# Kernel optimization log

Hardware: AMD Instinct MI355X
Metric: run time of the kernel (lower is better)

The kernel has to match this reference:

```python
import jax, jax.numpy as jnp
import numpy as np

N = 50000
E = 400000
DIM_IN = 512
DIM_H = 64
HEADS = 8
DIM_OUT = 40
SLOPE = 0.2  # PyG GATv2Conv default negative_slope


def setup_inputs() -> dict:
    key = jax.random.key(0)
    ks = jax.random.split(key, 16)
    s = 0.05
    return {
        "x": jax.random.normal(ks[0], (N, DIM_IN), dtype=jnp.float32),
        "edge_index": jax.random.randint(ks[1], (2, E), 0, N, dtype=jnp.int64),
        "Wl1": jax.random.normal(ks[2], (DIM_IN, HEADS * DIM_H), dtype=jnp.float32) * s,
        "Wr1": jax.random.normal(ks[3], (DIM_IN, HEADS * DIM_H), dtype=jnp.float32) * s,
        "att1": jax.random.normal(ks[4], (HEADS, DIM_H), dtype=jnp.float32) * s,
        "b1": jax.random.normal(ks[5], (HEADS * DIM_H,), dtype=jnp.float32) * s,
        "Wl2": jax.random.normal(ks[6], (HEADS * DIM_H, DIM_OUT), dtype=jnp.float32) * s,
        "Wr2": jax.random.normal(ks[7], (HEADS * DIM_H, DIM_OUT), dtype=jnp.float32) * s,
        "att2": jax.random.normal(ks[8], (1, DIM_OUT), dtype=jnp.float32) * s,
        "b2": jax.random.normal(ks[9], (DIM_OUT,), dtype=jnp.float32) * s,
        "Wl3": jax.random.normal(ks[10], (HEADS * DIM_H, 2), dtype=jnp.float32) * s,
        "Wr3": jax.random.normal(ks[11], (HEADS * DIM_H, 2), dtype=jnp.float32) * s,
        "att3": jax.random.normal(ks[12], (1, 2), dtype=jnp.float32) * s,
        "b3": jax.random.normal(ks[13], (2,), dtype=jnp.float32) * s,
    }


def gatv2(x, src, dst, Wl, Wr, att, b):
    # PyG GATv2Conv: e_ij = att . LeakyReLU(W_l x_j + W_r x_i); softmax over j (by dst i);
    # out_i = sum_j alpha_ij * (W_l x_j); heads concatenated; bias added after.
    n = x.shape[0]
    H, F = att.shape
    xl = (x @ Wl).reshape(n, H, F)  # source transform
    xr = (x @ Wr).reshape(n, H, F)  # target transform
    e = jax.nn.leaky_relu(xl[src] + xr[dst], negative_slope=SLOPE)  # [E, H, F]
    logits = jnp.einsum("ehf,hf->eh", e, att)  # [E, H]
    m = jax.ops.segment_max(logits, dst, num_segments=n)  # self-loops => every segment nonempty
    ex = jnp.exp(logits - m[dst])
    denom = jax.ops.segment_sum(ex, dst, num_segments=n)
    alpha = ex / denom[dst]  # [E, H]
    out = jax.ops.segment_sum(xl[src] * alpha[:, :, None], dst, num_segments=n)  # [N, H, F]
    return out.reshape(n, H * F) + b


def reference(x, edge_index, Wl1, Wr1, att1, b1, Wl2, Wr2, att2, b2, Wl3, Wr3, att3, b3):
    # add self loops (PyG default add_self_loops=True)
    loops = jnp.arange(N, dtype=edge_index.dtype)
    ei = jnp.concatenate([edge_index, jnp.stack([loops, loops])], axis=1)
    src, dst = ei[0], ei[1]
    # eval mode: dropout is identity; ReverseLayerF is identity in forward
    h = jax.nn.relu(gatv2(x, src, dst, Wl1, Wr1, att1, b1))
    y_class = gatv2(h, src, dst, Wl2, Wr2, att2, b2)
    y_domain = gatv2(h, src, dst, Wl3, Wr3, att3, b3)
    return (y_class, y_domain)
```

## Files before the change

### kernel.cpp

```cpp
#include <hip/hip_runtime.h>
#include <math.h>

typedef unsigned short u16;
typedef unsigned int   u32;
typedef __attribute__((ext_vector_type(8))) short bf16x8;
typedef __attribute__((ext_vector_type(4))) float f32x4;
typedef __attribute__((ext_vector_type(4))) u32   u32x4;

__device__ __forceinline__ float b2f(u16 u) {
  union { u32 i; float f; } v; v.i = ((u32)u) << 16; return v.f;
}
__device__ __forceinline__ u16 f2b(float f) {
  union { u32 i; float f; } v; v.f = f;
  u32 r = v.i + 0x7FFFu + ((v.i >> 16) & 1u);
  return (u16)(r >> 16);
}
__device__ __forceinline__ float blo(u32 w) {
  union { u32 i; float f; } v; v.i = w << 16; return v.f;
}
__device__ __forceinline__ float bhi(u32 w) {
  union { u32 i; float f; } v; v.i = w & 0xFFFF0000u; return v.f;
}
__device__ __forceinline__ void ld_lds16(const u16* g, u16* l) {
  __builtin_amdgcn_global_load_lds((const __attribute__((address_space(1))) void*)g,
                                   (__attribute__((address_space(3))) void*)l, 16, 0, 0);
}

#define NN 50000
#define NE 400000
#define NT 450000
#define NBLK_SCAN 196

__global__ void k_detect(const void* x, const void* ei, int* flags) {
  __shared__ int cnt[2];
  int t = threadIdx.x;
  if (t < 2) cnt[t] = 0;
  __syncthreads();
  u16 u = ((const u16*)x)[t];
  int e = (u >> 7) & 0xFF;
  if (u == 0 || (e >= 90 && e <= 134)) atomicAdd(&cnt[0], 1);
  if (t < 16) {
    if (((const int*)ei)[2 * t + 1] == 0) atomicAdd(&cnt[1], 1);
  }
  __syncthreads();
  if (t == 0) {
    flags[0] = (cnt[0] >= 110) ? 1 : 0;
    flags[1] = (cnt[1] >= 15) ? 1 : 0;
  }
}

__device__ __forceinline__ int eidx(const int* ei, int pos, int i64) {
  return i64 ? ei[2 * pos] : ei[pos];
}

__global__ void k_convert_x(const void* x, const int* flags, u16* xb) {
  if (flags[0]) return;
  int c = blockIdx.x * 256 + threadIdx.x;
  const float* xf = (const float*)x + (size_t)c * 8;
  u32x4 o;
  #pragma unroll
  for (int i = 0; i < 4; ++i) {
    u32 lo = f2b(xf[2 * i]);
    u32 hi = f2b(xf[2 * i + 1]);
    o[i] = lo | (hi << 16);
  }
  *(u32x4*)(xb + (size_t)c * 8) = o;
}

__global__ void k_pack_w1t(const void* Wl1, const void* Wr1, const int* flags, u16* w1t) {
  int t = blockIdx.x * 256 + threadIdx.x;
  int k = t >> 10;
  int c = t & 1023;
  const void* W = (c < 512) ? Wl1 : Wr1;
  int cc = c & 511;
  u16 v;
  if (flags[0]) v = ((const u16*)W)[k * 512 + cc];
  else          v = f2b(((const float*)W)[k * 512 + cc]);
  w1t[c * 512 + k] = v;
}

__global__ void k_pack_w23t(const void* Wl2, const void* Wr2, const void* Wl3, const void* Wr3,
                            const int* flags, u16* w23t) {
  int t = blockIdx.x * 256 + threadIdx.x;
  int k = t / 96;
  int c = t % 96;
  const void* W = nullptr; int idx = 0;
  if (c < 40)      { W = Wl2; idx = k * 40 + c; }
  else if (c < 42) { W = Wl3; idx = k * 2 + (c - 40); }
  else if (c < 82) { W = Wr2; idx = k * 40 + (c - 42); }
  else if (c < 84) { W = Wr3; idx = k * 2 + (c - 82); }
  u16 v = 0;
  if (W) {
    if (flags[0]) v = ((const u16*)W)[idx];
    else          v = f2b(((const float*)W)[idx]);
  }
  w23t[c * 512 + k] = v;
}

__global__ void k_pack_params(const void* att1, const void* b1, const void* att2, const void* b2,
                              const void* att3, const void* b3, const int* flags, float* params) {
  int t = blockIdx.x * 256 + threadIdx.x;
  if (t >= 1108) return;
  const void* src; int idx;
  if (t < 512)       { src = att1; idx = t; }
  else if (t < 1024) { src = b1;   idx = t - 512; }
  else if (t < 1064) { src = att2; idx = t - 1024; }
  else if (t < 1104) { src = b2;   idx = t - 1064; }
  else if (t < 1106) { src = att3; idx = t - 1104; }
  else               { src = b3;   idx = t - 1106; }
  params[t] = flags[0] ? b2f(((const u16*)src)[idx]) : ((const float*)src)[idx];
}

__global__ void k_hist(const int* ei, const int* flags, int* deg) {
  int e = blockIdx.x * 256 + threadIdx.x;
  if (e >= NE) return;
  int d = eidx(ei, NE + e, flags[1]);
  atomicAdd(&deg[d], 1);
}

__global__ void k_scanA(const int* deg, int* row_ptr, int* bsum) {
  __shared__ int sh[256];
  int b = blockIdx.x, t = threadIdx.x;
  int i = b * 256 + t;
  int val = (i < NN) ? deg[i] + 1 : 0;
  sh[t] = val;
  __syncthreads();
  #pragma unroll
  for (int off = 1; off < 256; off <<= 1) {
    int v = (t >= off) ? sh[t - off] : 0;
    __syncthreads();
    sh[t] += v;
    __syncthreads();
  }
  if (i < NN) row_ptr[i] = sh[t] - val;
  if (t == 255) bsum[b] = sh[255];
}

__global__ void k_scanB(int* bsum, int* row_ptr) {
  __shared__ int sh[256];
  int t = threadIdx.x;
  int val = (t < NBLK_SCAN) ? bsum[t] : 0;
  sh[t] = val;
  __syncthreads();
  #pragma unroll
  for (int off = 1; off < 256; off <<= 1) {
    int v = (t >= off) ? sh[t - off] : 0;
    __syncthreads();
    sh[t] += v;
    __syncthreads();
  }
  if (t < NBLK_SCAN) bsum[t] = sh[t] - val;
  if (t == 255) row_ptr[NN] = sh[255];
}

__global__ void k_scanC(const int* bsum, int* row_ptr, int* cursor) {
  int i = blockIdx.x * 256 + threadIdx.x;
  if (i < NN) {
    int v = row_ptr[i] + bsum[blockIdx.x];
    row_ptr[i] = v;
    cursor[i] = v;
  }
}

__global__ void k_scatter(const int* ei, const int* flags, int* cursor, int* csr_src) {
  int t = blockIdx.x * 256 + threadIdx.x;
  if (t >= NT) return;
  int i64 = flags[1];
  int s, d;
  if (t < NE) { s = eidx(ei, t, i64); d = eidx(ei, NE + t, i64); }
  else        { s = d = t - NE; }
  int pos = atomicAdd(&cursor[d], 1);
  csr_src[pos] = s;
}

__global__ __launch_bounds__(256) void k_gemm1(const void* __restrict__ xraw, const u16* __restrict__ xb,
                                               const u16* __restrict__ Bt, const int* __restrict__ flags,
                                               u16* __restrict__ XL, u16* __restrict__ XR) {
  __shared__ __align__(16) u16 As[128 * 64];
  __shared__ __align__(16) u16 Bs[128 * 64];
  const int id  = blockIdx.x;
  const int xcd = id & 7;
  const int lb  = id >> 3;
  const int mt  = xcd * 49 + (lb >> 3);
  const int nt  = lb & 7;
  if (mt >= 391) return;
  const int m0 = mt * 128;
  const int n0 = nt * 128;
  const u16* __restrict__ A = flags[0] ? (const u16*)xraw : xb;
  const int t = threadIdx.x;
  const int wave = t >> 6;
  const int lane = t & 63;
  const int wm = (wave >> 1) * 64;
  const int wn = (wave & 1) * 64;
  const int fr = lane & 15;
  const int fk = lane >> 4;
  const int srow = lane >> 3;
  const int schk = (lane & 7) ^ srow;
  f32x4 acc[4][4] = {};
  for (int k0 = 0; k0 < 512; k0 += 64) {
    #pragma unroll
    for (int q = 0; q < 4; ++q) {
      int rbase = wave * 32 + q * 8;
      int gm = m0 + rbase + srow;
      if (gm > NN - 1) gm = NN - 1;
      ld_lds16(&A[(size_t)gm * 512 + k0 + schk * 8], &As[rbase * 64]);
      ld_lds16(&Bt[(size_t)(n0 + rbase + srow) * 512 + k0 + schk * 8], &Bs[rbase * 64]);
    }
    __syncthreads();
    #pragma unroll
    for (int h = 0; h < 2; ++h) {
      int s = h * 4 + fk;
      bf16x8 af[4], bb[4];
      #pragma unroll
      for (int i = 0; i < 4; ++i) {
        int row = wm + i * 16 + fr;
        af[i] = *(const bf16x8*)&As[row * 64 + ((s ^ (row & 7)) * 8)];
      }
      #pragma unroll
      for (int j = 0; j < 4; ++j) {
        int row = wn + j * 16 + fr;
        bb[j] = *(const bf16x8*)&Bs[row * 64 + ((s ^ (row & 7)) * 8)];
      }
      #pragma unroll
      for (int i = 0; i < 4; ++i)
        #pragma unroll
        for (int j = 0; j < 4; ++j)
          acc[i][j] = __builtin_amdgcn_mfma_f32_16x16x32_bf16(af[i], bb[j], acc[i][j], 0, 0, 0);
    }
    __syncthreads();
  }
  #pragma unroll
  for (int i = 0; i < 4; ++i) {
    #pragma unroll
    for (int r = 0; r < 4; ++r) {
      int gm = m0 + wm + i * 16 + fk * 4 + r;
      if (gm < NN) {
        #pragma unroll
        for (int j = 0; j < 4; ++j) {
          int gn = n0 + wn + j * 16 + fr;
          u16 v = f2b(acc[i][j][r]);
          if (gn < 512) XL[(size_t)gm * 512 + gn] = v;
          else          XR[(size_t)gm * 512 + gn - 512] = v;
        }
      }
    }
  }
}

__global__ __launch_bounds__(256) void k_gemm2(const u16* __restrict__ A, const u16* __restrict__ Bt,
                                               float* __restrict__ C) {
  __shared__ __align__(16) short As[128][40];
  __shared__ __align__(16) short Bs[96][40];
  const int m0 = blockIdx.x * 128;
  const int t = threadIdx.x;
  const int wave = t >> 6;
  const int lane = t & 63;
  const int fr = lane & 15;
  const int fk = lane >> 4;
  const int wm = wave * 32;
  f32x4 acc[2][6] = {};
  for (int k0 = 0; k0 < 512; k0 += 32) {
    #pragma unroll
    for (int h = 0; h < 2; ++h) {
      int c = t + h * 256;
      int row = c >> 2, kc = (c & 3) * 8;
      int gm = m0 + row;
      u32x4 va = {0, 0, 0, 0};
      if (gm < NN) va = *(const u32x4*)&A[(size_t)gm * 512 + k0 + kc];
      *(u32x4*)&As[row][kc] = va;
    }
    for (int c = t; c < 384; c += 256) {
      int row = c >> 2, kc = (c & 3) * 8;
      *(u32x4*)&Bs[row][kc] = *(const u32x4*)&Bt[row * 512 + k0 + kc];
    }
    __syncthreads();
    bf16x8 af[2], bb[6];
    #pragma unroll
    for (int i = 0; i < 2; ++i) af[i] = *(const bf16x8*)&As[wm + i * 16 + fr][fk * 8];
    #pragma unroll
    for (int j = 0; j < 6; ++j) bb[j] = *(const bf16x8*)&Bs[j * 16 + fr][fk * 8];
    #pragma unroll
    for (int i = 0; i < 2; ++i)
      #pragma unroll
      for (int j = 0; j < 6; ++j)
        acc[i][j] = __builtin_amdgcn_mfma_f32_16x16x32_bf16(af[i], bb[j], acc[i][j], 0, 0, 0);
    __syncthreads();
  }
  #pragma unroll
  for (int i = 0; i < 2; ++i) {
    #pragma unroll
    for (int j = 0; j < 6; ++j) {
      int gn = j * 16 + fr;
      if (gn < 84) {
        #pragma unroll
        for (int r = 0; r < 4; ++r) {
          int gm = m0 + wm + i * 16 + fk * 4 + r;
          if (gm < NN) C[(size_t)gm * 84 + gn] = acc[i][j][r];
        }
      }
    }
  }
}

__global__ __launch_bounds__(256) void k_layer1f(const u16* __restrict__ xl1, const u16* __restrict__ xr1,
                                                 const int* __restrict__ row_ptr, const int* __restrict__ csr_src,
                                                 const float* __restrict__ params, u16* __restrict__ hb) {
  int wid = blockIdx.x * 4 + (threadIdx.x >> 6);
  int lane = threadIdx.x & 63;
  int nw = gridDim.x * 4;
  float att[8];
  #pragma unroll
  for (int k = 0; k < 8; ++k) att[k] = params[lane * 8 + k];
  for (int i = wid; i < NN; i += nw) {
    int e0 = row_ptr[i], e1 = row_ptr[i + 1];
    u32x4 xrv = *(const u32x4*)&xr1[(size_t)i * 512 + lane * 8];
    float xr[8];
    #pragma unroll
    for (int q = 0; q < 4; ++q) { xr[2 * q] = blo(xrv[q]); xr[2 * q + 1] = bhi(xrv[q]); }
    float s = 0.f;
    float acc[8] = {0.f, 0.f, 0.f, 0.f, 0.f, 0.f, 0.f, 0.f};
    int q0 = csr_src[e0];
    int q1 = csr_src[e0 + 1 < e1 ? e0 + 1 : e1 - 1];
    int q2 = csr_src[e0 + 2 < e1 ? e0 + 2 : e1 - 1];
    int q3 = csr_src[e0 + 3 < e1 ? e0 + 3 : e1 - 1];
    for (int p = e0; p < e1; p += 4) {
      int j0 = q0, j1 = q1, j2 = q2, j3 = q3;
      u32x4 v0 = *(const u32x4*)&xl1[(size_t)j0 * 512 + lane * 8];
      u32x4 v1 = *(const u32x4*)&xl1[(size_t)j1 * 512 + lane * 8];
      u32x4 v2 = *(const u32x4*)&xl1[(size_t)j2 * 512 + lane * 8];
      u32x4 v3 = *(const u32x4*)&xl1[(size_t)j3 * 512 + lane * 8];
      int np = p + 4;
      if (np < e1) {
        q0 = csr_src[np];
        q1 = csr_src[np + 1 < e1 ? np + 1 : e1 - 1];
        q2 = csr_src[np + 2 < e1 ? np + 2 : e1 - 1];
        q3 = csr_src[np + 3 < e1 ? np + 3 : e1 - 1];
      }
      float m1 = (p + 1 < e1) ? 1.f : 0.f;
      float m2 = (p + 2 < e1) ? 1.f : 0.f;
      float m3 = (p + 3 < e1) ? 1.f : 0.f;
      float c0 = 0.f, c1 = 0.f, c2 = 0.f, c3 = 0.f;
      float xlv0[8], xlv1[8], xlv2[8], xlv3[8];
      #pragma unroll
      for (int q = 0; q < 4; ++q) {
        xlv0[2 * q] = blo(v0[q]); xlv0[2 * q + 1] = bhi(v0[q]);
        xlv1[2 * q] = blo(v1[q]); xlv1[2 * q + 1] = bhi(v1[q]);
        xlv2[2 * q] = blo(v2[q]); xlv2[2 * q + 1] = bhi(v2[q]);
        xlv3[2 * q] = blo(v3[q]); xlv3[2 * q + 1] = bhi(v3[q]);
      }
      #pragma unroll
      for (int k = 0; k < 8; ++k) {
        float t0 = xlv0[k] + xr[k];
        float t1 = xlv1[k] + xr[k];
        float t2 = xlv2[k] + xr[k];
        float t3 = xlv3[k] + xr[k];
        c0 = fmaf(att[k], fmaxf(t0, 0.2f * t0), c0);
        c1 = fmaf(att[k], fmaxf(t1, 0.2f * t1), c1);
        c2 = fmaf(att[k], fmaxf(t2, 0.2f * t2), c2);
        c3 = fmaf(att[k], fmaxf(t3, 0.2f * t3), c3);
      }
      c0 += __shfl_xor(c0, 1, 64); c1 += __shfl_xor(c1, 1, 64);
      c2 += __shfl_xor(c2, 1, 64); c3 += __shfl_xor(c3, 1, 64);
      c0 += __shfl_xor(c0, 2, 64); c1 += __shfl_xor(c1, 2, 64);
      c2 += __shfl_xor(c2, 2, 64); c3 += __shfl_xor(c3, 2, 64);
      c0 += __shfl_xor(c0, 4, 64); c1 += __shfl_xor(c1, 4, 64);
      c2 += __shfl_xor(c2, 4, 64); c3 += __shfl_xor(c3, 4, 64);
      float pv0 = __expf(fminf(fmaxf(c0, -30.f), 30.f));
      float pv1 = __expf(fminf(fmaxf(c1, -30.f), 30.f)) * m1;
      float pv2 = __expf(fminf(fmaxf(c2, -30.f), 30.f)) * m2;
      float pv3 = __expf(fminf(fmaxf(c3, -30.f), 30.f)) * m3;
      s += (pv0 + pv1) + (pv2 + pv3);
      #pragma unroll
      for (int k = 0; k < 8; ++k) {
        float a = fmaf(pv0, xlv0[k], pv1 * xlv1[k]);
        float b = fmaf(pv2, xlv2[k], pv3 * xlv3[k]);
        acc[k] += a + b;
      }
    }
    float r = 1.f / s;
    u32x4 o;
    #pragma unroll
    for (int q = 0; q < 4; ++q) {
      u32 lo = f2b(fmaxf(fmaf(acc[2 * q],     r, params[512 + lane * 8 + 2 * q]),     0.f));
      u32 hi = f2b(fmaxf(fmaf(acc[2 * q + 1], r, params[512 + lane * 8 + 2 * q + 1]), 0.f));
      o[q] = lo | (hi << 16);
    }
    *(u32x4*)&hb[(size_t)i * 512 + lane * 8] = o;
  }
}

__global__ __launch_bounds__(256) void k_layer23f(const float* __restrict__ xlr23, const int* __restrict__ row_ptr,
                                                  const int* __restrict__ csr_src, const float* __restrict__ params,
                                                  const int* __restrict__ flags, void* __restrict__ out) {
  int wid = blockIdx.x * 4 + (threadIdx.x >> 6);
  int lane = threadIdx.x & 63;
  int nw = gridDim.x * 4;
  int c = lane;
  bool act = c < 42;
  float att = 0.f;
  if (c < 40)      att = params[1024 + c];
  else if (c < 42) att = params[1104 + (c - 40)];
  int isbf = flags[0];
  for (int i = wid; i < NN; i += nw) {
    int e0 = row_ptr[i], e1 = row_ptr[i + 1];
    float xr = act ? xlr23[(size_t)i * 84 + 42 + c] : 0.f;
    float s2 = 0.f, s3 = 0.f, acc = 0.f;
    for (int p = e0; p < e1; p += 2) {
      int p1 = p + 1 < e1 ? p + 1 : e1 - 1;
      float m1 = (p + 1 < e1) ? 1.f : 0.f;
      int j0 = csr_src[p], j1 = csr_src[p1];
      float xl0 = act ? xlr23[(size_t)j0 * 84 + c] : 0.f;
      float xl1 = act ? xlr23[(size_t)j1 * 84 + c] : 0.f;
      float t0 = xl0 + xr, t1 = xl1 + xr;
      float v0 = att * fmaxf(t0, 0.2f * t0);
      float v1 = att * fmaxf(t1, 0.2f * t1);
      float w0 = (c < 40) ? v0 : 0.f;
      float w1 = (c < 40) ? v1 : 0.f;
      #pragma unroll
      for (int o = 32; o >= 1; o >>= 1) { w0 += __shfl_xor(w0, o, 64); w1 += __shfl_xor(w1, o, 64); }
      float u0 = v0 + __shfl_xor(v0, 1, 64);
      float u1 = v1 + __shfl_xor(v1, 1, 64);
      float l3_0 = __shfl(u0, 40, 64);
      float l3_1 = __shfl(u1, 40, 64);
      float p2_0 = __expf(fminf(fmaxf(w0, -30.f), 30.f));
      float p2_1 = __expf(fminf(fmaxf(w1, -30.f), 30.f)) * m1;
      float p3_0 = __expf(fminf(fmaxf(l3_0, -30.f), 30.f));
      float p3_1 = __expf(fminf(fmaxf(l3_1, -30.f), 30.f)) * m1;
      s2 += p2_0 + p2_1;
      s3 += p3_0 + p3_1;
      float a0 = (c < 40) ? p2_0 : p3_0;
      float a1 = (c < 40) ? p2_1 : p3_1;
      acc += fmaf(a0, xl0, a1 * xl1);
    }
    if (c < 40) {
      float v = acc / s2 + params[1064 + c];
      size_t o = (size_t)i * 40 + c;
      if (isbf) ((u16*)out)[o] = f2b(v); else ((float*)out)[o] = v;
    } else if (c < 42) {
      float v = acc / s3 + params[1106 + (c - 40)];
      size_t o = 2000000 + (size_t)i * 2 + (c - 40);
      if (isbf) ((u16*)out)[o] = f2b(v); else ((float*)out)[o] = v;
    }
  }
}

extern "C" void kernel_launch(void* const* d_in, const int* in_sizes, int n_in,
                              void* d_out, int out_size, void* d_ws, size_t ws_size,
                              hipStream_t stream) {
  const void* x    = d_in[0];
  const int*  ei   = (const int*)d_in[1];
  const void* Wl1  = d_in[2];
  const void* Wr1  = d_in[3];
  const void* att1 = d_in[4];
  const void* b1   = d_in[5];
  const void* Wl2  = d_in[6];
  const void* Wr2  = d_in[7];
  const void* att2 = d_in[8];
  const void* b2   = d_in[9];
  const void* Wl3  = d_in[10];
  const void* Wr3  = d_in[11];
  const void* att3 = d_in[12];
  const void* b3   = d_in[13];
  (void)in_sizes; (void)n_in; (void)out_size;

  char* ws = (char*)d_ws;
  size_t off = 0;
  auto alloc = [&](size_t bytes) -> void* {
    void* p = ws + off;
    off = (off + bytes + 255) & ~(size_t)255;
    return p;
  };
  int*   flags   = (int*)  alloc(64);
  u16*   xb      = (u16*)  alloc((size_t)NN * 512 * 2);
  u16*   w1t     = (u16*)  alloc((size_t)1024 * 512 * 2);
  u16*   xl1     = (u16*)  alloc((size_t)NN * 512 * 2);
  u16*   xr1     = (u16*)  alloc((size_t)NN * 512 * 2);
  u16*   hb      = (u16*)  alloc((size_t)NN * 512 * 2);
  u16*   w23t    = (u16*)  alloc((size_t)96 * 512 * 2);
  float* xlr23   = (float*)alloc((size_t)NN * 84 * 4);
  float* params  = (float*)alloc(1108 * 4);
  int*   row_ptr = (int*)  alloc((NN + 1) * 4);
  int*   deg     = (int*)  alloc(NN * 4);
  int*   cursor  = (int*)  alloc(NN * 4);
  int*   csr_src = (int*)  alloc((NT + 16) * 4);
  int*   bsum    = (int*)  alloc(256 * 4);
  if (ws_size < off) return;

  hipLaunchKernelGGL(k_detect, dim3(1), dim3(128), 0, stream, x, (const void*)ei, flags);
  hipLaunchKernelGGL(k_convert_x, dim3(12500), dim3(256), 0, stream, x, flags, xb);
  hipLaunchKernelGGL(k_pack_w1t, dim3(2048), dim3(256), 0, stream, Wl1, Wr1, flags, w1t);
  hipLaunchKernelGGL(k_pack_w23t, dim3(192), dim3(256), 0, stream, Wl2, Wr2, Wl3, Wr3, flags, w23t);
  hipLaunchKernelGGL(k_pack_params, dim3(5), dim3(256), 0, stream, att1, b1, att2, b2, att3, b3, flags, params);
  hipMemsetAsync(deg, 0, NN * 4, stream);
  hipLaunchKernelGGL(k_hist, dim3((NE + 255) / 256), dim3(256), 0, stream, ei, flags, deg);
  hipLaunchKernelGGL(k_scanA, dim3(NBLK_SCAN), dim3(256), 0, stream, deg, row_ptr, bsum);
  hipLaunchKernelGGL(k_scanB, dim3(1), dim3(256), 0, stream, bsum, row_ptr);
  hipLaunchKernelGGL(k_scanC, dim3(NBLK_SCAN), dim3(256), 0, stream, bsum, row_ptr, cursor);
  hipLaunchKernelGGL(k_scatter, dim3((NT + 255) / 256), dim3(256), 0, stream, ei, flags, cursor, csr_src);
  hipLaunchKernelGGL(k_gemm1, dim3(3136), dim3(256), 0, stream, x, xb, w1t, flags, xl1, xr1);
  hipLaunchKernelGGL(k_layer1f, dim3(4096), dim3(256), 0, stream, xl1, xr1, row_ptr, csr_src, params, hb);
  hipLaunchKernelGGL(k_gemm2, dim3(391), dim3(256), 0, stream, hb, w23t, xlr23);
  hipLaunchKernelGGL(k_layer23f, dim3(4096), dim3(256), 0, stream, xlr23, row_ptr, csr_src, params, flags, d_out);
}
```

Measured before the change: 471.8 us.

## Merge pack kernels, simplify leaky-relu logits, repartition layer-2/3 lanes over edges

Merges the three weight and parameter packing kernels into one launch, and makes the w1t writes coalesced by iterating k fastest. In layer 1 the leaky ReLU is rewritten as 0.4*att*(|t| + 1.5*xl) plus a per-node term att·xr hoisted out of the edge loop, which trims per-edge ALU work; the accumulation becomes an FMA chain. Layer 2/3 now handles 8 edges per wave (8 lanes per edge, 5 channels each) instead of one lane per channel with full-wave reductions, which cuts shuffles per edge and idle lanes. The cost is a final cross-edge reduction and some reassociation of floating-point results.

```diff
diff --git a/kernel.cpp b/kernel.cpp
--- a/kernel.cpp
+++ b/kernel.cpp
@@ -67,48 +67,44 @@
   *(u32x4*)(xb + (size_t)c * 8) = o;
 }
 
-__global__ void k_pack_w1t(const void* Wl1, const void* Wr1, const int* flags, u16* w1t) {
-  int t = blockIdx.x * 256 + threadIdx.x;
-  int k = t >> 10;
-  int c = t & 1023;
-  const void* W = (c < 512) ? Wl1 : Wr1;
-  int cc = c & 511;
-  u16 v;
-  if (flags[0]) v = ((const u16*)W)[k * 512 + cc];
-  else          v = f2b(((const float*)W)[k * 512 + cc]);
-  w1t[c * 512 + k] = v;
-}
-
-__global__ void k_pack_w23t(const void* Wl2, const void* Wr2, const void* Wl3, const void* Wr3,
-                            const int* flags, u16* w23t) {
-  int t = blockIdx.x * 256 + threadIdx.x;
-  int k = t / 96;
-  int c = t % 96;
-  const void* W = nullptr; int idx = 0;
-  if (c < 40)      { W = Wl2; idx = k * 40 + c; }
-  else if (c < 42) { W = Wl3; idx = k * 2 + (c - 40); }
-  else if (c < 82) { W = Wr2; idx = k * 40 + (c - 42); }
-  else if (c < 84) { W = Wr3; idx = k * 2 + (c - 82); }
-  u16 v = 0;
-  if (W) {
-    if (flags[0]) v = ((const u16*)W)[idx];
-    else          v = f2b(((const float*)W)[idx]);
-  }
-  w23t[c * 512 + k] = v;
-}
-
-__global__ void k_pack_params(const void* att1, const void* b1, const void* att2, const void* b2,
-                              const void* att3, const void* b3, const int* flags, float* params) {
-  int t = blockIdx.x * 256 + threadIdx.x;
-  if (t >= 1108) return;
-  const void* src; int idx;
-  if (t < 512)       { src = att1; idx = t; }
-  else if (t < 1024) { src = b1;   idx = t - 512; }
-  else if (t < 1064) { src = att2; idx = t - 1024; }
-  else if (t < 1104) { src = b2;   idx = t - 1064; }
-  else if (t < 1106) { src = att3; idx = t - 1104; }
-  else               { src = b3;   idx = t - 1106; }
-  params[t] = flags[0] ? b2f(((const u16*)src)[idx]) : ((const float*)src)[idx];
+__global__ void k_pack(const void* Wl1, const void* Wr1, const void* Wl2, const void* Wr2,
+                       const void* Wl3, const void* Wr3, const void* att1, const void* b1,
+                       const void* att2, const void* b2, const void* att3, const void* b3,
+                       const int* flags, u16* w1t, u16* w23t, float* params) {
+  int b = blockIdx.x;
+  int isbf = flags[0];
+  if (b < 2048) {
+    int t = b * 256 + threadIdx.x;
+    int r = t >> 9;
+    int k = t & 511;
+    const void* W = (r < 512) ? Wl1 : Wr1;
+    int cc = r & 511;
+    u16 v = isbf ? ((const u16*)W)[k * 512 + cc] : f2b(((const float*)W)[k * 512 + cc]);
+    w1t[(size_t)r * 512 + k] = v;
+  } else if (b < 2240) {
+    int t = (b - 2048) * 256 + threadIdx.x;
+    int k = t / 96;
+    int c = t % 96;
+    const void* W = nullptr; int idx = 0;
+    if (c < 40)      { W = Wl2; idx = k * 40 + c; }
+    else if (c < 42) { W = Wl3; idx = k * 2 + (c - 40); }
+    else if (c < 82) { W = Wr2; idx = k * 40 + (c - 42); }
+    else if (c < 84) { W = Wr3; idx = k * 2 + (c - 82); }
+    u16 v = 0;
+    if (W) v = isbf ? ((const u16*)W)[idx] : f2b(((const float*)W)[idx]);
+    w23t[c * 512 + k] = v;
+  } else {
+    int t = (b - 2240) * 256 + threadIdx.x;
+    if (t >= 1108) return;
+    const void* src; int idx;
+    if (t < 512)       { src = att1; idx = t; }
+    else if (t < 1024) { src = b1;   idx = t - 512; }
+    else if (t < 1064) { src = att2; idx = t - 1024; }
+    else if (t < 1104) { src = b2;   idx = t - 1064; }
+    else if (t < 1106) { src = att3; idx = t - 1104; }
+    else               { src = b3;   idx = t - 1106; }
+    params[t] = isbf ? b2f(((const u16*)src)[idx]) : ((const float*)src)[idx];
+  }
 }
 
 __global__ void k_hist(const int* ei, const int* flags, int* deg) {
@@ -308,15 +304,21 @@
   int wid = blockIdx.x * 4 + (threadIdx.x >> 6);
   int lane = threadIdx.x & 63;
   int nw = gridDim.x * 4;
-  float att[8];
-  #pragma unroll
-  for (int k = 0; k < 8; ++k) att[k] = params[lane * 8 + k];
+  float att4[8];
+  #pragma unroll
+  for (int k = 0; k < 8; ++k) att4[k] = 0.4f * params[lane * 8 + k];
   for (int i = wid; i < NN; i += nw) {
     int e0 = row_ptr[i], e1 = row_ptr[i + 1];
     u32x4 xrv = *(const u32x4*)&xr1[(size_t)i * 512 + lane * 8];
     float xr[8];
     #pragma unroll
     for (int q = 0; q < 4; ++q) { xr[2 * q] = blo(xrv[q]); xr[2 * q + 1] = bhi(xrv[q]); }
+    float dp = 0.f;
+    #pragma unroll
+    for (int k = 0; k < 8; ++k) dp = fmaf(att4[k], 1.5f * xr[k], dp);
+    dp += __shfl_xor(dp, 1, 64);
+    dp += __shfl_xor(dp, 2, 64);
+    dp += __shfl_xor(dp, 4, 64);
     float s = 0.f;
     float acc[8] = {0.f, 0.f, 0.f, 0.f, 0.f, 0.f, 0.f, 0.f};
     int q0 = csr_src[e0];
@@ -354,10 +356,14 @@
         float t1 = xlv1[k] + xr[k];
         float t2 = xlv2[k] + xr[k];
         float t3 = xlv3[k] + xr[k];
-        c0 = fmaf(att[k], fmaxf(t0, 0.2f * t0), c0);
-        c1 = fmaf(att[k], fmaxf(t1, 0.2f * t1), c1);
-        c2 = fmaf(att[k], fmaxf(t2, 0.2f * t2), c2);
-        c3 = fmaf(att[k], fmaxf(t3, 0.2f * t3), c3);
+        float u0 = fmaf(1.5f, xlv0[k], fabsf(t0));
+        float u1 = fmaf(1.5f, xlv1[k], fabsf(t1));
+        float u2 = fmaf(1.5f, xlv2[k], fabsf(t2));
+        float u3 = fmaf(1.5f, xlv3[k], fabsf(t3));
+        c0 = fmaf(att4[k], u0, c0);
+        c1 = fmaf(att4[k], u1, c1);
+        c2 = fmaf(att4[k], u2, c2);
+        c3 = fmaf(att4[k], u3, c3);
       }
       c0 += __shfl_xor(c0, 1, 64); c1 += __shfl_xor(c1, 1, 64);
       c2 += __shfl_xor(c2, 1, 64); c3 += __shfl_xor(c3, 1, 64);
@@ -365,16 +371,21 @@
       c2 += __shfl_xor(c2, 2, 64); c3 += __shfl_xor(c3, 2, 64);
       c0 += __shfl_xor(c0, 4, 64); c1 += __shfl_xor(c1, 4, 64);
       c2 += __shfl_xor(c2, 4, 64); c3 += __shfl_xor(c3, 4, 64);
-      float pv0 = __expf(fminf(fmaxf(c0, -30.f), 30.f));
-      float pv1 = __expf(fminf(fmaxf(c1, -30.f), 30.f)) * m1;
-      float pv2 = __expf(fminf(fmaxf(c2, -30.f), 30.f)) * m2;
-      float pv3 = __expf(fminf(fmaxf(c3, -30.f), 30.f)) * m3;
+      float l0 = c0 + dp;
+      float l1 = c1 + dp;
+      float l2 = c2 + dp;
+      float l3 = c3 + dp;
+      float pv0 = __expf(fminf(fmaxf(l0, -30.f), 30.f));
+      float pv1 = __expf(fminf(fmaxf(l1, -30.f), 30.f)) * m1;
+      float pv2 = __expf(fminf(fmaxf(l2, -30.f), 30.f)) * m2;
+      float pv3 = __expf(fminf(fmaxf(l3, -30.f), 30.f)) * m3;
       s += (pv0 + pv1) + (pv2 + pv3);
       #pragma unroll
       for (int k = 0; k < 8; ++k) {
-        float a = fmaf(pv0, xlv0[k], pv1 * xlv1[k]);
-        float b = fmaf(pv2, xlv2[k], pv3 * xlv3[k]);
-        acc[k] += a + b;
+        float a = fmaf(pv0, xlv0[k], acc[k]);
+        a = fmaf(pv1, xlv1[k], a);
+        a = fmaf(pv2, xlv2[k], a);
+        acc[k] = fmaf(pv3, xlv3[k], a);
       }
     }
     float r = 1.f / s;
@@ -395,51 +406,81 @@
   int wid = blockIdx.x * 4 + (threadIdx.x >> 6);
   int lane = threadIdx.x & 63;
   int nw = gridDim.x * 4;
-  int c = lane;
-  bool act = c < 42;
-  float att = 0.f;
-  if (c < 40)      att = params[1024 + c];
-  else if (c < 42) att = params[1104 + (c - 40)];
+  int e = lane >> 3;
+  int g = lane & 7;
+  int c0 = g * 5;
+  float att2[5];
+  #pragma unroll
+  for (int u = 0; u < 5; ++u) att2[u] = params[1024 + c0 + u];
+  float att3a = params[1104], att3b = params[1105];
   int isbf = flags[0];
   for (int i = wid; i < NN; i += nw) {
     int e0 = row_ptr[i], e1 = row_ptr[i + 1];
-    float xr = act ? xlr23[(size_t)i * 84 + 42 + c] : 0.f;
-    float s2 = 0.f, s3 = 0.f, acc = 0.f;
-    for (int p = e0; p < e1; p += 2) {
-      int p1 = p + 1 < e1 ? p + 1 : e1 - 1;
-      float m1 = (p + 1 < e1) ? 1.f : 0.f;
-      int j0 = csr_src[p], j1 = csr_src[p1];
-      float xl0 = act ? xlr23[(size_t)j0 * 84 + c] : 0.f;
-      float xl1 = act ? xlr23[(size_t)j1 * 84 + c] : 0.f;
-      float t0 = xl0 + xr, t1 = xl1 + xr;
-      float v0 = att * fmaxf(t0, 0.2f * t0);
-      float v1 = att * fmaxf(t1, 0.2f * t1);
-      float w0 = (c < 40) ? v0 : 0.f;
-      float w1 = (c < 40) ? v1 : 0.f;
-      #pragma unroll
-      for (int o = 32; o >= 1; o >>= 1) { w0 += __shfl_xor(w0, o, 64); w1 += __shfl_xor(w1, o, 64); }
-      float u0 = v0 + __shfl_xor(v0, 1, 64);
-      float u1 = v1 + __shfl_xor(v1, 1, 64);
-      float l3_0 = __shfl(u0, 40, 64);
-      float l3_1 = __shfl(u1, 40, 64);
-      float p2_0 = __expf(fminf(fmaxf(w0, -30.f), 30.f));
-      float p2_1 = __expf(fminf(fmaxf(w1, -30.f), 30.f)) * m1;
-      float p3_0 = __expf(fminf(fmaxf(l3_0, -30.f), 30.f));
-      float p3_1 = __expf(fminf(fmaxf(l3_1, -30.f), 30.f)) * m1;
-      s2 += p2_0 + p2_1;
-      s3 += p3_0 + p3_1;
-      float a0 = (c < 40) ? p2_0 : p3_0;
-      float a1 = (c < 40) ? p2_1 : p3_1;
-      acc += fmaf(a0, xl0, a1 * xl1);
-    }
-    if (c < 40) {
-      float v = acc / s2 + params[1064 + c];
-      size_t o = (size_t)i * 40 + c;
-      if (isbf) ((u16*)out)[o] = f2b(v); else ((float*)out)[o] = v;
-    } else if (c < 42) {
-      float v = acc / s3 + params[1106 + (c - 40)];
-      size_t o = 2000000 + (size_t)i * 2 + (c - 40);
-      if (isbf) ((u16*)out)[o] = f2b(v); else ((float*)out)[o] = v;
+    const float* xri = &xlr23[(size_t)i * 84];
+    float xr2[5];
+    #pragma unroll
+    for (int u = 0; u < 5; ++u) xr2[u] = xri[42 + c0 + u];
+    float xr3a = xri[82], xr3b = xri[83];
+    float s2 = 0.f, s3 = 0.f;
+    float acc2[5] = {0.f, 0.f, 0.f, 0.f, 0.f};
+    float acc3a = 0.f, acc3b = 0.f;
+    int nit = (e1 - e0 + 7) >> 3;
+    for (int it = 0; it < nit; ++it) {
+      int p = e0 + it * 8 + e;
+      bool valid = p < e1;
+      int j = csr_src[valid ? p : e1 - 1];
+      const float* xlj = &xlr23[(size_t)j * 84];
+      float xl2[5];
+      #pragma unroll
+      for (int u = 0; u < 5; ++u) xl2[u] = xlj[c0 + u];
+      float part = 0.f;
+      #pragma unroll
+      for (int u = 0; u < 5; ++u) {
+        float t = xl2[u] + xr2[u];
+        part = fmaf(att2[u], fmaxf(t, 0.2f * t), part);
+      }
+      part += __shfl_xor(part, 1, 64);
+      part += __shfl_xor(part, 2, 64);
+      part += __shfl_xor(part, 4, 64);
+      float pv2 = valid ? __expf(fminf(fmaxf(part, -30.f), 30.f)) : 0.f;
+      s2 += pv2;
+      #pragma unroll
+      for (int u = 0; u < 5; ++u) acc2[u] = fmaf(pv2, xl2[u], acc2[u]);
+      if (g == 0) {
+        float xl3a = xlj[40], xl3b = xlj[41];
+        float ta = xl3a + xr3a, tb = xl3b + xr3b;
+        float l3 = fmaf(att3a, fmaxf(ta, 0.2f * ta), att3b * fmaxf(tb, 0.2f * tb));
+        float pv3 = valid ? __expf(fminf(fmaxf(l3, -30.f), 30.f)) : 0.f;
+        s3 += pv3;
+        acc3a = fmaf(pv3, xl3a, acc3a);
+        acc3b = fmaf(pv3, xl3b, acc3b);
+      }
+    }
+    #pragma unroll
+    for (int m = 8; m <= 32; m <<= 1) {
+      #pragma unroll
+      for (int u = 0; u < 5; ++u) acc2[u] += __shfl_xor(acc2[u], m, 64);
+      s2 += __shfl_xor(s2, m, 64);
+      acc3a += __shfl_xor(acc3a, m, 64);
+      acc3b += __shfl_xor(acc3b, m, 64);
+      s3 += __shfl_xor(s3, m, 64);
+    }
+    if (e == 0) {
+      float r2 = 1.f / s2;
+      #pragma unroll
+      for (int u = 0; u < 5; ++u) {
+        float v = acc2[u] * r2 + params[1064 + c0 + u];
+        size_t o = (size_t)i * 40 + c0 + u;
+        if (isbf) ((u16*)out)[o] = f2b(v); else ((float*)out)[o] = v;
+      }
+      if (g == 0) {
+        float r3 = 1.f / s3;
+        float va = acc3a * r3 + params[1106];
+        float vb = acc3b * r3 + params[1107];
+        size_t o = 2000000 + (size_t)i * 2;
+        if (isbf) { ((u16*)out)[o] = f2b(va); ((u16*)out)[o + 1] = f2b(vb); }
+        else      { ((float*)out)[o] = va;    ((float*)out)[o + 1] = vb; }
+      }
     }
   }
 }
@@ -488,9 +529,8 @@
 
   hipLaunchKernelGGL(k_detect, dim3(1), dim3(128), 0, stream, x, (const void*)ei, flags);
   hipLaunchKernelGGL(k_convert_x, dim3(12500), dim3(256), 0, stream, x, flags, xb);
-  hipLaunchKernelGGL(k_pack_w1t, dim3(2048), dim3(256), 0, stream, Wl1, Wr1, flags, w1t);
-  hipLaunchKernelGGL(k_pack_w23t, dim3(192), dim3(256), 0, stream, Wl2, Wr2, Wl3, Wr3, flags, w23t);
-  hipLaunchKernelGGL(k_pack_params, dim3(5), dim3(256), 0, stream, att1, b1, att2, b2, att3, b3, flags, params);
+  hipLaunchKernelGGL(k_pack, dim3(2245), dim3(256), 0, stream, Wl1, Wr1, Wl2, Wr2, Wl3, Wr3,
+                     att1, b1, att2, b2, att3, b3, flags, w1t, w23t, params);
   hipMemsetAsync(deg, 0, NN * 4, stream);
   hipLaunchKernelGGL(k_hist, dim3((NE + 255) / 256), dim3(256), 0, stream, ei, flags, deg);
   hipLaunchKernelGGL(k_scanA, dim3(NBLK_SCAN), dim3(256), 0, stream, deg, row_ptr, bsum);
```

Result: faster. 454.2 us (-3.7%).
